# Performance work log

Measured on AMD Instinct MI355X. Metric: run time of the kernel, lower is better.

## Reference

```python
import jax, jax.numpy as jnp
import numpy as np

N = 50000   # active sparse voxels
B = 4       # batch size
FIN = 64
FOUT = 128
TEMB = 256
K = 27      # 3x3x3 kernel offsets
EPS = 1e-5


def _bn(x, gamma, beta, mean, var):
    # inference-style BatchNorm over channel dim
    return (x - mean) * jax.lax.rsqrt(var + EPS) * gamma + beta


def _sparse_conv(feats, nbr, mask, W):
    # submanifold sparse conv via kernel map:
    # out[n] = sum_k mask[k,n] * feats[nbr[k,n]] @ W[k]
    g = feats[nbr] * mask[..., None].astype(feats.dtype)   # [K, N, Fin]
    return jnp.einsum('knf,kfo->no', g, W)                  # [N, Fout]


def _make_kernel_map(k_nbr, k_msk, n):
    nbr = jax.random.randint(k_nbr, (K, N), 0, n, dtype=jnp.int32)
    mask = jax.random.bernoulli(k_msk, 0.4, (K, N))
    # center offset is the identity map and always valid (submanifold conv)
    nbr = nbr.at[K // 2].set(jnp.arange(N, dtype=jnp.int32))
    mask = mask.at[K // 2].set(True)
    return nbr, mask


def setup_inputs() -> dict:
    key = jax.random.key(0)
    ks = jax.random.split(key, 20)
    x_feats = jax.random.normal(ks[0], (N, FIN), jnp.float32)
    batch_idx = jax.random.randint(ks[1], (N,), 0, B, dtype=jnp.int32)
    t = jax.random.normal(ks[2], (B, TEMB), jnp.float32)
    nbr1, mask1 = _make_kernel_map(ks[3], ks[4], N)
    nbr2, mask2 = _make_kernel_map(ks[5], ks[6], N)
    s1 = 1.0 / np.sqrt(FIN * K)
    s2 = 1.0 / np.sqrt(FOUT * K)
    return {
        'x_feats': x_feats, 'batch_idx': batch_idx, 't': t,
        'nbr1': nbr1, 'mask1': mask1, 'nbr2': nbr2, 'mask2': mask2,
        'bn1_gamma': jnp.ones((FIN,), jnp.float32),
        'bn1_beta': jnp.zeros((FIN,), jnp.float32),
        'bn1_mean': 0.1 * jax.random.normal(ks[7], (FIN,), jnp.float32),
        'bn1_var': jax.random.uniform(ks[8], (FIN,), jnp.float32, 0.5, 1.5),
        'W1': s1 * jax.random.normal(ks[9], (K, FIN, FOUT), jnp.float32),
        't_W': (1.0 / np.sqrt(TEMB)) * jax.random.normal(ks[10], (TEMB, FOUT), jnp.float32),
        't_b': jnp.zeros((FOUT,), jnp.float32),
        'bn2_gamma': jnp.ones((FOUT,), jnp.float32),
        'bn2_beta': jnp.zeros((FOUT,), jnp.float32),
        'bn2_mean': 0.1 * jax.random.normal(ks[11], (FOUT,), jnp.float32),
        'bn2_var': jax.random.uniform(ks[12], (FOUT,), jnp.float32, 0.5, 1.5),
        'W2': s2 * jax.random.normal(ks[13], (K, FOUT, FOUT), jnp.float32),
        'res_W': (1.0 / np.sqrt(FIN)) * jax.random.normal(ks[14], (FIN, FOUT), jnp.float32),
        'res_b': jnp.zeros((FOUT,), jnp.float32),
    }


def reference(x_feats, batch_idx, t, nbr1, mask1, nbr2, mask2,
              bn1_gamma, bn1_beta, bn1_mean, bn1_var, W1,
              t_W, t_b,
              bn2_gamma, bn2_beta, bn2_mean, bn2_var, W2,
              res_W, res_b):
    # conv1 block: BN -> SiLU -> sparse Conv3d
    h = jax.nn.silu(_bn(x_feats, bn1_gamma, bn1_beta, bn1_mean, bn1_var))
    h = _sparse_conv(h, nbr1, mask1, W1)                      # [N, FOUT]
    # FiLM-style time embedding, broadcast per point via batch index
    t_emb = jax.nn.silu(t) @ t_W + t_b                        # [B, FOUT]
    h = h + t_emb[batch_idx]
    # conv2 block
    h2 = jax.nn.silu(_bn(h, bn2_gamma, bn2_beta, bn2_mean, bn2_var))
    h2 = _sparse_conv(h2, nbr2, mask2, W2)                    # [N, FOUT]
    # residual connection (f_in != f_out -> Linear)
    return h2 + (x_feats @ res_W + res_b)
```

## Files before the change

### kernel.cpp

```cpp
#include <hip/hip_runtime.h>


#define EPS 1e-5f

typedef __attribute__((ext_vector_type(8))) short s16x8;
typedef __attribute__((ext_vector_type(4))) float f32x4;
typedef __attribute__((ext_vector_type(4))) unsigned short u16x4;

static __device__ __forceinline__ unsigned short f2bf(float f) {
    union { float f; unsigned u; } v; v.f = f;
    unsigned r = v.u + 0x7fffu + ((v.u >> 16) & 1u);
    return (unsigned short)(r >> 16);
}
static __device__ __forceinline__ float silu_d(float x) {
    return x / (1.f + __expf(-x));
}
static __device__ __forceinline__ void gload_lds16(const void* gsrc, void* ldst) {
    __builtin_amdgcn_global_load_lds(
        (const __attribute__((address_space(1))) unsigned int*)gsrc,
        (__attribute__((address_space(3))) unsigned int*)ldst, 16, 0, 0);
}
static __device__ __forceinline__ int mask_shift(const unsigned char* mask, int NV) {
    size_t base = (size_t)13 * (size_t)NV;
    int v = ((base & 3) == 3) ? 2 : 1;
    return (mask[base + v] == 1) ? 0 : 2;
}

__global__ void k_prep_small(const float* __restrict__ t, const float* __restrict__ tW,
                             const float* __restrict__ tb,
                             const float* __restrict__ g2, const float* __restrict__ b2,
                             const float* __restrict__ m2, const float* __restrict__ v2,
                             float* __restrict__ temb, float* __restrict__ sc,
                             float* __restrict__ sh, int B) {
    int tid = threadIdx.x;
    if (tid < B * 128) {
        int b = tid >> 7, o = tid & 127;
        float s = 0.f;
        for (int e = 0; e < 256; ++e) {
            float tv = t[b * 256 + e];
            s += silu_d(tv) * tW[e * 128 + o];
        }
        temb[tid] = s + tb[o];
    }
    if (tid < 128) {
        float rstd = rsqrtf(v2[tid] + EPS);
        float s1 = g2[tid] * rstd;
        sc[tid] = s1;
        sh[tid] = b2[tid] - m2[tid] * s1;
    }
}

__global__ __launch_bounds__(256) void k_shuffle(
        const float* __restrict__ W1, const float* __restrict__ W2,
        const float* __restrict__ rW,
        unsigned short* __restrict__ W1s, unsigned short* __restrict__ W2s,
        unsigned short* __restrict__ rWs) {
    int tid = blockIdx.x * 256 + threadIdx.x;
    const int n1 = 432 * 512, n2 = 864 * 512, n3 = 16 * 512;
    if (tid < n1) {
        int f = tid >> 9, r = tid & 511, lane = r >> 3, j = r & 7;
        int mt = f & 7, fk = f >> 3, ks = fk & 1, ko = fk >> 1;
        int fin = ks * 32 + (lane >> 4) * 8 + j;
        int fout = mt * 16 + (lane & 15);
        W1s[tid] = f2bf(W1[(ko * 64 + fin) * 128 + fout]);
    } else if (tid < n1 + n2) {
        int e = tid - n1;
        int f = e >> 9, r = e & 511, lane = r >> 3, j = r & 7;
        int mt = f & 7, fk = f >> 3, ks = fk & 3, ko = fk >> 2;
        int fin = ks * 32 + (lane >> 4) * 8 + j;
        int fout = mt * 16 + (lane & 15);
        W2s[e] = f2bf(W2[(ko * 128 + fin) * 128 + fout]);
    } else if (tid < n1 + n2 + n3) {
        int e = tid - n1 - n2;
        int f = e >> 9, r = e & 511, lane = r >> 3, j = r & 7;
        int mt = f & 7, ks = f >> 3;
        int fin = ks * 32 + (lane >> 4) * 8 + j;
        int fout = mt * 16 + (lane & 15);
        rWs[e] = f2bf(rW[fin * 128 + fout]);
    }
}

__global__ __launch_bounds__(256) void k_elem(
        const float* __restrict__ x,
        const float* __restrict__ g1, const float* __restrict__ b1,
        const float* __restrict__ m1, const float* __restrict__ v1,
        unsigned short* __restrict__ h1, int NV) {
    int tid = blockIdx.x * 256 + threadIdx.x;
    if (tid >= NV * 16) return;
    int n = tid >> 4, c = (tid & 15) << 2;
    f32x4 xv = *(const f32x4*)(x + n * 64 + c);
    f32x4 gv = *(const f32x4*)(g1 + c);
    f32x4 bv = *(const f32x4*)(b1 + c);
    f32x4 mv = *(const f32x4*)(m1 + c);
    f32x4 vv = *(const f32x4*)(v1 + c);
    u16x4 ho;
#pragma unroll
    for (int j = 0; j < 4; ++j) {
        float xn = (xv[j] - mv[j]) * rsqrtf(vv[j] + EPS) * gv[j] + bv[j];
        ho[j] = f2bf(silu_d(xn));
    }
    *(u16x4*)(h1 + n * 64 + c) = ho;
}

__global__ __launch_bounds__(512) void k_conv1(
        const unsigned short* __restrict__ h1, const int* __restrict__ nbr,
        const unsigned char* __restrict__ mask, const unsigned short* __restrict__ W1s,
        const float* __restrict__ temb, const int* __restrict__ bidx,
        const float* __restrict__ bn2sc, const float* __restrict__ bn2sh,
        unsigned short* __restrict__ h2in, int NV) {
    __shared__ unsigned short lds0[8192];
    __shared__ unsigned short lds1[8192];
    const int lane = threadIdx.x & 63;
    const int wave = threadIdx.x >> 6;
    const int g = lane >> 4, col = lane & 15;
    const int v = blockIdx.x * 128 + wave * 16 + col;
    const bool vok = v < NV;
    const int msh = mask_shift(mask, NV);

    f32x4 acc[8];
    const f32x4 z4 = {0.f, 0.f, 0.f, 0.f};
#pragma unroll
    for (int m = 0; m < 8; ++m) acc[m] = z4;
    const s16x8 zz = {0, 0, 0, 0, 0, 0, 0, 0};

    auto loadr = [&](int t) -> int {
        if (!vok) return -1;
        int off = t * NV + v;
        int nv = nbr[off];
        bool mm = mask[(size_t)off << msh] != 0;
        return mm ? nv : -1;
    };

    {
        const char* src = (const char*)W1s + (size_t)threadIdx.x * 16;
        char* dst = (char*)lds0 + (size_t)threadIdx.x * 16;
#pragma unroll
        for (int i = 0; i < 2; ++i)
            gload_lds16(src + i * 8192, dst + i * 8192);
    }
    int rA = loadr(0);
    int rN = loadr(1);
    int r0 = rA < 0 ? 0 : rA;
    s16x8 p0 = *(const s16x8*)(h1 + r0 * 64 + 0 * 32 + g * 8);
    s16x8 p1 = *(const s16x8*)(h1 + r0 * 64 + 1 * 32 + g * 8);
    __syncthreads();

    unsigned short* bufc = lds0;
    unsigned short* bufn = lds1;

    for (int t = 0; t < 27; ++t) {
        s16x8 q0, q1;
        int rN2 = -1;
        if (t < 26) {
            const char* src = (const char*)W1s + (size_t)(t + 1) * 16384 + (size_t)threadIdx.x * 16;
            char* dst = (char*)bufn + (size_t)threadIdx.x * 16;
#pragma unroll
            for (int i = 0; i < 2; ++i)
                gload_lds16(src + i * 8192, dst + i * 8192);
            int rn = rN < 0 ? 0 : rN;
            q0 = *(const s16x8*)(h1 + rn * 64 + 0 * 32 + g * 8);
            q1 = *(const s16x8*)(h1 + rn * 64 + 1 * 32 + g * 8);
        }
        if (t < 25) rN2 = loadr(t + 2);
        const bool m = rA >= 0;
        s16x8 b0 = m ? p0 : zz;
        s16x8 b1 = m ? p1 : zz;
        const unsigned short* wp = bufc + lane * 8;
#pragma unroll
        for (int mt = 0; mt < 8; ++mt) {
            s16x8 a = *(const s16x8*)(wp + (0 * 8 + mt) * 512);
            acc[mt] = __builtin_amdgcn_mfma_f32_16x16x32_bf16(a, b0, acc[mt], 0, 0, 0);
        }
#pragma unroll
        for (int mt = 0; mt < 8; ++mt) {
            s16x8 a = *(const s16x8*)(wp + (1 * 8 + mt) * 512);
            acc[mt] = __builtin_amdgcn_mfma_f32_16x16x32_bf16(a, b1, acc[mt], 0, 0, 0);
        }
        if (t < 26) {
            __syncthreads();
            p0 = q0; p1 = q1;
            rA = rN; rN = rN2;
            unsigned short* tmp = bufc; bufc = bufn; bufn = tmp;
        }
    }

    if (vok) {
        int b = bidx[v];
        const float* te = temb + b * 128;
#pragma unroll
        for (int mt = 0; mt < 8; ++mt) {
            int c = mt * 16 + g * 4;
            f32x4 val = acc[mt];
            f32x4 tv = *(const f32x4*)(te + c);
            f32x4 sc = *(const f32x4*)(bn2sc + c);
            f32x4 sh = *(const f32x4*)(bn2sh + c);
            u16x4 o;
#pragma unroll
            for (int j = 0; j < 4; ++j) {
                float zv = (val[j] + tv[j]) * sc[j] + sh[j];
                o[j] = f2bf(silu_d(zv));
            }
            *(u16x4*)(h2in + v * 128 + c) = o;
        }
    }
}

__global__ __launch_bounds__(512) void k_conv2(
        const unsigned short* __restrict__ h2in, const int* __restrict__ nbr,
        const unsigned char* __restrict__ mask, const unsigned short* __restrict__ W2s,
        const float* __restrict__ x, const unsigned short* __restrict__ rWs,
        const float* __restrict__ resb, float* __restrict__ out, int NV) {
    __shared__ unsigned short lds0[8192];
    __shared__ unsigned short lds1[8192];
    const int lane = threadIdx.x & 63;
    const int wave = threadIdx.x >> 6;
    const int g = lane >> 4, col = lane & 15;
    const int v = blockIdx.x * 128 + wave * 16 + col;
    const bool vok = v < NV;
    const int msh = mask_shift(mask, NV);

    f32x4 acc[8];
    const f32x4 z4 = {0.f, 0.f, 0.f, 0.f};
#pragma unroll
    for (int m = 0; m < 8; ++m) acc[m] = z4;
    const s16x8 zz = {0, 0, 0, 0, 0, 0, 0, 0};

    auto loadr = [&](int t) -> int {
        if (!vok) return -1;
        int off = t * NV + v;
        int nv = nbr[off];
        bool mm = mask[(size_t)off << msh] != 0;
        return mm ? nv : -1;
    };

    {
        const char* src = (const char*)W2s + (size_t)threadIdx.x * 16;
        char* dst = (char*)lds0 + (size_t)threadIdx.x * 16;
#pragma unroll
        for (int i = 0; i < 2; ++i)
            gload_lds16(src + i * 8192, dst + i * 8192);
    }
    int rA = loadr(0);
    int rN = loadr(1);
    int r0 = rA < 0 ? 0 : rA;
    s16x8 pA0 = *(const s16x8*)(h2in + r0 * 128 + 0 * 32 + g * 8);
    s16x8 pA1 = *(const s16x8*)(h2in + r0 * 128 + 1 * 32 + g * 8);
    s16x8 pB0 = *(const s16x8*)(h2in + r0 * 128 + 2 * 32 + g * 8);
    s16x8 pB1 = *(const s16x8*)(h2in + r0 * 128 + 3 * 32 + g * 8);

    {
        int rv = vok ? v : 0;
#pragma unroll
        for (int ks = 0; ks < 2; ++ks) {
            f32x4 xa = *(const f32x4*)(x + rv * 64 + ks * 32 + g * 8);
            f32x4 xb = *(const f32x4*)(x + rv * 64 + ks * 32 + g * 8 + 4);
            s16x8 b;
#pragma unroll
            for (int j = 0; j < 4; ++j) {
                b[j]     = (short)f2bf(xa[j]);
                b[j + 4] = (short)f2bf(xb[j]);
            }
            const unsigned short* wp = rWs + ks * 4096 + lane * 8;
#pragma unroll
            for (int mt = 0; mt < 8; ++mt) {
                s16x8 a = *(const s16x8*)(wp + mt * 512);
                acc[mt] = __builtin_amdgcn_mfma_f32_16x16x32_bf16(a, b, acc[mt], 0, 0, 0);
            }
        }
    }
    __syncthreads();

    for (int t = 0; t < 27; ++t) {
        const bool m = rA >= 0;
        const int rn = rN < 0 ? 0 : rN;
        s16x8 qA0, qA1, qB0, qB1;
        int rN2 = -1;

        {
            const char* src = (const char*)W2s + ((size_t)t * 2 + 1) * 16384 + (size_t)threadIdx.x * 16;
            char* dst = (char*)lds1 + (size_t)threadIdx.x * 16;
#pragma unroll
            for (int i = 0; i < 2; ++i)
                gload_lds16(src + i * 8192, dst + i * 8192);
            if (t < 26) {
                qA0 = *(const s16x8*)(h2in + rn * 128 + 0 * 32 + g * 8);
                qA1 = *(const s16x8*)(h2in + rn * 128 + 1 * 32 + g * 8);
            }
            if (t < 25) rN2 = loadr(t + 2);
            s16x8 b0 = m ? pA0 : zz;
            s16x8 b1 = m ? pA1 : zz;
            const unsigned short* wp = lds0 + lane * 8;
#pragma unroll
            for (int mt = 0; mt < 8; ++mt) {
                s16x8 a = *(const s16x8*)(wp + (0 * 8 + mt) * 512);
                acc[mt] = __builtin_amdgcn_mfma_f32_16x16x32_bf16(a, b0, acc[mt], 0, 0, 0);
            }
#pragma unroll
            for (int mt = 0; mt < 8; ++mt) {
                s16x8 a = *(const s16x8*)(wp + (1 * 8 + mt) * 512);
                acc[mt] = __builtin_amdgcn_mfma_f32_16x16x32_bf16(a, b1, acc[mt], 0, 0, 0);
            }
            __syncthreads();
        }

        {
            if (t < 26) {
                const char* src = (const char*)W2s + ((size_t)(t + 1) * 2 + 0) * 16384 + (size_t)threadIdx.x * 16;
                char* dst = (char*)lds0 + (size_t)threadIdx.x * 16;
#pragma unroll
                for (int i = 0; i < 2; ++i)
                    gload_lds16(src + i * 8192, dst + i * 8192);
                qB0 = *(const s16x8*)(h2in + rn * 128 + 2 * 32 + g * 8);
                qB1 = *(const s16x8*)(h2in + rn * 128 + 3 * 32 + g * 8);
            }
            s16x8 b0 = m ? pB0 : zz;
            s16x8 b1 = m ? pB1 : zz;
            const unsigned short* wp = lds1 + lane * 8;
#pragma unroll
            for (int mt = 0; mt < 8; ++mt) {
                s16x8 a = *(const s16x8*)(wp + (0 * 8 + mt) * 512);
                acc[mt] = __builtin_amdgcn_mfma_f32_16x16x32_bf16(a, b0, acc[mt], 0, 0, 0);
            }
#pragma unroll
            for (int mt = 0; mt < 8; ++mt) {
                s16x8 a = *(const s16x8*)(wp + (1 * 8 + mt) * 512);
                acc[mt] = __builtin_amdgcn_mfma_f32_16x16x32_bf16(a, b1, acc[mt], 0, 0, 0);
            }
            __syncthreads();
        }

        pA0 = qA0; pA1 = qA1; pB0 = qB0; pB1 = qB1;
        rA = rN; rN = rN2;
    }

    if (vok) {
#pragma unroll
        for (int mt = 0; mt < 8; ++mt) {
            int c = mt * 16 + g * 4;
            f32x4 rr = acc[mt] + *(const f32x4*)(resb + c);
            *(f32x4*)(out + v * 128 + c) = rr;
        }
    }
}

extern "C" void kernel_launch(void* const* d_in, const int* in_sizes, int n_in,
                              void* d_out, int out_size, void* d_ws, size_t ws_size,
                              hipStream_t stream) {
    const float* x          = (const float*)d_in[0];
    const int* bidx         = (const int*)d_in[1];
    const float* t          = (const float*)d_in[2];
    const int* nbr1         = (const int*)d_in[3];
    const unsigned char* mask1 = (const unsigned char*)d_in[4];
    const int* nbr2         = (const int*)d_in[5];
    const unsigned char* mask2 = (const unsigned char*)d_in[6];
    const float* bn1g       = (const float*)d_in[7];
    const float* bn1b       = (const float*)d_in[8];
    const float* bn1m       = (const float*)d_in[9];
    const float* bn1v       = (const float*)d_in[10];
    const float* W1         = (const float*)d_in[11];
    const float* tW         = (const float*)d_in[12];
    const float* tb         = (const float*)d_in[13];
    const float* bn2g       = (const float*)d_in[14];
    const float* bn2b       = (const float*)d_in[15];
    const float* bn2m       = (const float*)d_in[16];
    const float* bn2v       = (const float*)d_in[17];
    const float* W2         = (const float*)d_in[18];
    const float* rW         = (const float*)d_in[19];
    const float* resb       = (const float*)d_in[20];

    const int NV = in_sizes[0] / 64;
    const int B  = in_sizes[2] / 256;
    float* out = (float*)d_out;

    char* ws = (char*)d_ws;
    size_t o_W1s = 0;
    size_t o_W2s = o_W1s + (size_t)432 * 1024;
    size_t o_rWs = o_W2s + (size_t)864 * 1024;
    size_t o_te  = o_rWs + (size_t)16 * 1024;
    size_t o_sc  = o_te  + (size_t)B * 128 * 4;
    size_t o_sh  = o_sc  + 512;
    size_t o_h1  = o_sh  + 512;
    size_t o_h2  = o_h1  + (size_t)NV * 64 * 2;

    unsigned short* W1s  = (unsigned short*)(ws + o_W1s);
    unsigned short* W2s  = (unsigned short*)(ws + o_W2s);
    unsigned short* rWs  = (unsigned short*)(ws + o_rWs);
    float* temb  = (float*)(ws + o_te);
    float* bn2sc = (float*)(ws + o_sc);
    float* bn2sh = (float*)(ws + o_sh);
    unsigned short* h1   = (unsigned short*)(ws + o_h1);
    unsigned short* h2in = (unsigned short*)(ws + o_h2);

    k_prep_small<<<1, 512, 0, stream>>>(t, tW, tb, bn2g, bn2b, bn2m, bn2v,
                                        temb, bn2sc, bn2sh, B);
    {
        int total = (432 + 864 + 16) * 512;
        int grid = (total + 255) / 256;
        k_shuffle<<<grid, 256, 0, stream>>>(W1, W2, rW, W1s, W2s, rWs);
    }
    {
        int total = NV * 16;
        int grid = (total + 255) / 256;
        k_elem<<<grid, 256, 0, stream>>>(x, bn1g, bn1b, bn1m, bn1v, h1, NV);
    }
    {
        int grid = (NV + 127) / 128;
        k_conv1<<<grid, 512, 0, stream>>>(h1, nbr1, mask1, W1s, temb, bidx,
                                          bn2sc, bn2sh, h2in, NV);
        k_conv2<<<grid, 512, 0, stream>>>(h2in, nbr2, mask2, W2s, x, rWs,
                                          resb, out, NV);
    }
}
```

Measured before the change: 143.2 us.

## Split output channels across two blocks per voxel tile in sparse convs

Each 128-voxel tile is now handled by two blocks, each computing one 64-channel half of the output. The shuffled weight layout is reordered so each half's weights are contiguous, which halves per-block LDS weight traffic and accumulator registers. In conv2 the per-offset K loop is restructured into a single double-buffered stage per offset instead of two half-stages. The goal is more blocks and higher occupancy. The cost is that the neighbor index, mask and feature gathers are duplicated across the two blocks.

Result: slower. 199.3 us (+39.2%).

```diff
diff --git a/kernel.cpp b/kernel.cpp
--- a/kernel.cpp
+++ b/kernel.cpp
@@ -59,16 +59,18 @@
     const int n1 = 432 * 512, n2 = 864 * 512, n3 = 16 * 512;
     if (tid < n1) {
         int f = tid >> 9, r = tid & 511, lane = r >> 3, j = r & 7;
-        int mt = f & 7, fk = f >> 3, ks = fk & 1, ko = fk >> 1;
+        int w = f & 7, mtl = w & 3, ks = w >> 2;
+        int chunk = f >> 3, h = chunk & 1, ko = chunk >> 1;
         int fin = ks * 32 + (lane >> 4) * 8 + j;
-        int fout = mt * 16 + (lane & 15);
+        int fout = h * 64 + mtl * 16 + (lane & 15);
         W1s[tid] = f2bf(W1[(ko * 64 + fin) * 128 + fout]);
     } else if (tid < n1 + n2) {
         int e = tid - n1;
         int f = e >> 9, r = e & 511, lane = r >> 3, j = r & 7;
-        int mt = f & 7, fk = f >> 3, ks = fk & 3, ko = fk >> 2;
+        int w = f & 15, mtl = w & 3, ks = w >> 2;
+        int chunk = f >> 4, h = chunk & 1, ko = chunk >> 1;
         int fin = ks * 32 + (lane >> 4) * 8 + j;
-        int fout = mt * 16 + (lane & 15);
+        int fout = h * 64 + mtl * 16 + (lane & 15);
         W2s[e] = f2bf(W2[(ko * 128 + fin) * 128 + fout]);
     } else if (tid < n1 + n2 + n3) {
         int e = tid - n1 - n2;
@@ -108,19 +110,20 @@
         const float* __restrict__ temb, const int* __restrict__ bidx,
         const float* __restrict__ bn2sc, const float* __restrict__ bn2sh,
         unsigned short* __restrict__ h2in, int NV) {
-    __shared__ unsigned short lds0[8192];
-    __shared__ unsigned short lds1[8192];
+    __shared__ unsigned short lds0[4096];
+    __shared__ unsigned short lds1[4096];
+    const int vb = blockIdx.x >> 1, h = blockIdx.x & 1;
     const int lane = threadIdx.x & 63;
     const int wave = threadIdx.x >> 6;
     const int g = lane >> 4, col = lane & 15;
-    const int v = blockIdx.x * 128 + wave * 16 + col;
+    const int v = vb * 128 + wave * 16 + col;
     const bool vok = v < NV;
     const int msh = mask_shift(mask, NV);
 
-    f32x4 acc[8];
+    f32x4 acc[4];
     const f32x4 z4 = {0.f, 0.f, 0.f, 0.f};
 #pragma unroll
-    for (int m = 0; m < 8; ++m) acc[m] = z4;
+    for (int m = 0; m < 4; ++m) acc[m] = z4;
     const s16x8 zz = {0, 0, 0, 0, 0, 0, 0, 0};
 
     auto loadr = [&](int t) -> int {
@@ -132,11 +135,9 @@
     };
 
     {
-        const char* src = (const char*)W1s + (size_t)threadIdx.x * 16;
+        const char* src = (const char*)W1s + (size_t)h * 8192 + (size_t)threadIdx.x * 16;
         char* dst = (char*)lds0 + (size_t)threadIdx.x * 16;
-#pragma unroll
-        for (int i = 0; i < 2; ++i)
-            gload_lds16(src + i * 8192, dst + i * 8192);
+        gload_lds16(src, dst);
     }
     int rA = loadr(0);
     int rN = loadr(1);
@@ -152,11 +153,9 @@
         s16x8 q0, q1;
         int rN2 = -1;
         if (t < 26) {
-            const char* src = (const char*)W1s + (size_t)(t + 1) * 16384 + (size_t)threadIdx.x * 16;
+            const char* src = (const char*)W1s + ((size_t)(t + 1) * 2 + h) * 8192 + (size_t)threadIdx.x * 16;
             char* dst = (char*)bufn + (size_t)threadIdx.x * 16;
-#pragma unroll
-            for (int i = 0; i < 2; ++i)
-                gload_lds16(src + i * 8192, dst + i * 8192);
+            gload_lds16(src, dst);
             int rn = rN < 0 ? 0 : rN;
             q0 = *(const s16x8*)(h1 + rn * 64 + 0 * 32 + g * 8);
             q1 = *(const s16x8*)(h1 + rn * 64 + 1 * 32 + g * 8);
@@ -167,14 +166,14 @@
         s16x8 b1 = m ? p1 : zz;
         const unsigned short* wp = bufc + lane * 8;
 #pragma unroll
-        for (int mt = 0; mt < 8; ++mt) {
-            s16x8 a = *(const s16x8*)(wp + (0 * 8 + mt) * 512);
-            acc[mt] = __builtin_amdgcn_mfma_f32_16x16x32_bf16(a, b0, acc[mt], 0, 0, 0);
-        }
-#pragma unroll
-        for (int mt = 0; mt < 8; ++mt) {
-            s16x8 a = *(const s16x8*)(wp + (1 * 8 + mt) * 512);
-            acc[mt] = __builtin_amdgcn_mfma_f32_16x16x32_bf16(a, b1, acc[mt], 0, 0, 0);
+        for (int mtl = 0; mtl < 4; ++mtl) {
+            s16x8 a = *(const s16x8*)(wp + (0 * 4 + mtl) * 512);
+            acc[mtl] = __builtin_amdgcn_mfma_f32_16x16x32_bf16(a, b0, acc[mtl], 0, 0, 0);
+        }
+#pragma unroll
+        for (int mtl = 0; mtl < 4; ++mtl) {
+            s16x8 a = *(const s16x8*)(wp + (1 * 4 + mtl) * 512);
+            acc[mtl] = __builtin_amdgcn_mfma_f32_16x16x32_bf16(a, b1, acc[mtl], 0, 0, 0);
         }
         if (t < 26) {
             __syncthreads();
@@ -188,9 +187,9 @@
         int b = bidx[v];
         const float* te = temb + b * 128;
 #pragma unroll
-        for (int mt = 0; mt < 8; ++mt) {
-            int c = mt * 16 + g * 4;
-            f32x4 val = acc[mt];
+        for (int mtl = 0; mtl < 4; ++mtl) {
+            int c = h * 64 + mtl * 16 + g * 4;
+            f32x4 val = acc[mtl];
             f32x4 tv = *(const f32x4*)(te + c);
             f32x4 sc = *(const f32x4*)(bn2sc + c);
             f32x4 sh = *(const f32x4*)(bn2sh + c);
@@ -212,17 +211,18 @@
         const float* __restrict__ resb, float* __restrict__ out, int NV) {
     __shared__ unsigned short lds0[8192];
     __shared__ unsigned short lds1[8192];
+    const int vb = blockIdx.x >> 1, h = blockIdx.x & 1;
     const int lane = threadIdx.x & 63;
     const int wave = threadIdx.x >> 6;
     const int g = lane >> 4, col = lane & 15;
-    const int v = blockIdx.x * 128 + wave * 16 + col;
+    const int v = vb * 128 + wave * 16 + col;
     const bool vok = v < NV;
     const int msh = mask_shift(mask, NV);
 
-    f32x4 acc[8];
+    f32x4 acc[4];
     const f32x4 z4 = {0.f, 0.f, 0.f, 0.f};
 #pragma unroll
-    for (int m = 0; m < 8; ++m) acc[m] = z4;
+    for (int m = 0; m < 4; ++m) acc[m] = z4;
     const s16x8 zz = {0, 0, 0, 0, 0, 0, 0, 0};
 
     auto loadr = [&](int t) -> int {
@@ -234,7 +234,7 @@
     };
 
     {
-        const char* src = (const char*)W2s + (size_t)threadIdx.x * 16;
+        const char* src = (const char*)W2s + (size_t)h * 16384 + (size_t)threadIdx.x * 16;
         char* dst = (char*)lds0 + (size_t)threadIdx.x * 16;
 #pragma unroll
         for (int i = 0; i < 2; ++i)
@@ -243,10 +243,10 @@
     int rA = loadr(0);
     int rN = loadr(1);
     int r0 = rA < 0 ? 0 : rA;
-    s16x8 pA0 = *(const s16x8*)(h2in + r0 * 128 + 0 * 32 + g * 8);
-    s16x8 pA1 = *(const s16x8*)(h2in + r0 * 128 + 1 * 32 + g * 8);
-    s16x8 pB0 = *(const s16x8*)(h2in + r0 * 128 + 2 * 32 + g * 8);
-    s16x8 pB1 = *(const s16x8*)(h2in + r0 * 128 + 3 * 32 + g * 8);
+    s16x8 p0 = *(const s16x8*)(h2in + r0 * 128 + 0 * 32 + g * 8);
+    s16x8 p1 = *(const s16x8*)(h2in + r0 * 128 + 1 * 32 + g * 8);
+    s16x8 p2 = *(const s16x8*)(h2in + r0 * 128 + 2 * 32 + g * 8);
+    s16x8 p3 = *(const s16x8*)(h2in + r0 * 128 + 3 * 32 + g * 8);
 
     {
         int rv = vok ? v : 0;
@@ -260,84 +260,73 @@
                 b[j]     = (short)f2bf(xa[j]);
                 b[j + 4] = (short)f2bf(xb[j]);
             }
-            const unsigned short* wp = rWs + ks * 4096 + lane * 8;
-#pragma unroll
-            for (int mt = 0; mt < 8; ++mt) {
-                s16x8 a = *(const s16x8*)(wp + mt * 512);
-                acc[mt] = __builtin_amdgcn_mfma_f32_16x16x32_bf16(a, b, acc[mt], 0, 0, 0);
+#pragma unroll
+            for (int mtl = 0; mtl < 4; ++mtl) {
+                s16x8 a = *(const s16x8*)(rWs + (ks * 8 + h * 4 + mtl) * 512 + lane * 8);
+                acc[mtl] = __builtin_amdgcn_mfma_f32_16x16x32_bf16(a, b, acc[mtl], 0, 0, 0);
             }
         }
     }
     __syncthreads();
 
+    unsigned short* bufc = lds0;
+    unsigned short* bufn = lds1;
+
     for (int t = 0; t < 27; ++t) {
-        const bool m = rA >= 0;
-        const int rn = rN < 0 ? 0 : rN;
-        s16x8 qA0, qA1, qB0, qB1;
+        s16x8 q0, q1, q2, q3;
         int rN2 = -1;
-
-        {
-            const char* src = (const char*)W2s + ((size_t)t * 2 + 1) * 16384 + (size_t)threadIdx.x * 16;
-            char* dst = (char*)lds1 + (size_t)threadIdx.x * 16;
+        if (t < 26) {
+            const char* src = (const char*)W2s + ((size_t)(t + 1) * 2 + h) * 16384 + (size_t)threadIdx.x * 16;
+            char* dst = (char*)bufn + (size_t)threadIdx.x * 16;
 #pragma unroll
             for (int i = 0; i < 2; ++i)
                 gload_lds16(src + i * 8192, dst + i * 8192);
-            if (t < 26) {
-                qA0 = *(const s16x8*)(h2in + rn * 128 + 0 * 32 + g * 8);
-                qA1 = *(const s16x8*)(h2in + rn * 128 + 1 * 32 + g * 8);
-            }
-            if (t < 25) rN2 = loadr(t + 2);
-            s16x8 b0 = m ? pA0 : zz;
-            s16x8 b1 = m ? pA1 : zz;
-            const unsigned short* wp = lds0 + lane * 8;
-#pragma unroll
-            for (int mt = 0; mt < 8; ++mt) {
-                s16x8 a = *(const s16x8*)(wp + (0 * 8 + mt) * 512);
-                acc[mt] = __builtin_amdgcn_mfma_f32_16x16x32_bf16(a, b0, acc[mt], 0, 0, 0);
-            }
-#pragma unroll
-            for (int mt = 0; mt < 8; ++mt) {
-                s16x8 a = *(const s16x8*)(wp + (1 * 8 + mt) * 512);
-                acc[mt] = __builtin_amdgcn_mfma_f32_16x16x32_bf16(a, b1, acc[mt], 0, 0, 0);
-            }
+            int rn = rN < 0 ? 0 : rN;
+            q0 = *(const s16x8*)(h2in + rn * 128 + 0 * 32 + g * 8);
+            q1 = *(const s16x8*)(h2in + rn * 128 + 1 * 32 + g * 8);
+            q2 = *(const s16x8*)(h2in + rn * 128 + 2 * 32 + g * 8);
+            q3 = *(const s16x8*)(h2in + rn * 128 + 3 * 32 + g * 8);
+        }
+        if (t < 25) rN2 = loadr(t + 2);
+        const bool m = rA >= 0;
+        s16x8 b0 = m ? p0 : zz;
+        s16x8 b1 = m ? p1 : zz;
+        s16x8 b2 = m ? p2 : zz;
+        s16x8 b3 = m ? p3 : zz;
+        const unsigned short* wp = bufc + lane * 8;
+#pragma unroll
+        for (int mtl = 0; mtl < 4; ++mtl) {
+            s16x8 a = *(const s16x8*)(wp + (0 * 4 + mtl) * 512);
+            acc[mtl] = __builtin_amdgcn_mfma_f32_16x16x32_bf16(a, b0, acc[mtl], 0, 0, 0);
+        }
+#pragma unroll
+        for (int mtl = 0; mtl < 4; ++mtl) {
+            s16x8 a = *(const s16x8*)(wp + (1 * 4 + mtl) * 512);
+            acc[mtl] = __builtin_amdgcn_mfma_f32_16x16x32_bf16(a, b1, acc[mtl], 0, 0, 0);
+        }
+#pragma unroll
+        for (int mtl = 0; mtl < 4; ++mtl) {
+            s16x8 a = *(const s16x8*)(wp + (2 * 4 + mtl) * 512);
+            acc[mtl] = __builtin_amdgcn_mfma_f32_16x16x32_bf16(a, b2, acc[mtl], 0, 0, 0);
+        }
+#pragma unroll
+        for (int mtl = 0; mtl < 4; ++mtl) {
+            s16x8 a = *(const s16x8*)(wp + (3 * 4 + mtl) * 512);
+            acc[mtl] = __builtin_amdgcn_mfma_f32_16x16x32_bf16(a, b3, acc[mtl], 0, 0, 0);
+        }
+        if (t < 26) {
             __syncthreads();
-        }
-
-        {
-            if (t < 26) {
-                const char* src = (const char*)W2s + ((size_t)(t + 1) * 2 + 0) * 16384 + (size_t)threadIdx.x * 16;
-                char* dst = (char*)lds0 + (size_t)threadIdx.x * 16;
-#pragma unroll
-                for (int i = 0; i < 2; ++i)
-                    gload_lds16(src + i * 8192, dst + i * 8192);
-                qB0 = *(const s16x8*)(h2in + rn * 128 + 2 * 32 + g * 8);
-                qB1 = *(const s16x8*)(h2in + rn * 128 + 3 * 32 + g * 8);
-            }
-            s16x8 b0 = m ? pB0 : zz;
-            s16x8 b1 = m ? pB1 : zz;
-            const unsigned short* wp = lds1 + lane * 8;
-#pragma unroll
-            for (int mt = 0; mt < 8; ++mt) {
-                s16x8 a = *(const s16x8*)(wp + (0 * 8 + mt) * 512);
-                acc[mt] = __builtin_amdgcn_mfma_f32_16x16x32_bf16(a, b0, acc[mt], 0, 0, 0);
-            }
-#pragma unroll
-            for (int mt = 0; mt < 8; ++mt) {
-                s16x8 a = *(const s16x8*)(wp + (1 * 8 + mt) * 512);
-                acc[mt] = __builtin_amdgcn_mfma_f32_16x16x32_bf16(a, b1, acc[mt], 0, 0, 0);
-            }
-            __syncthreads();
-        }
-
-        pA0 = qA0; pA1 = qA1; pB0 = qB0; pB1 = qB1;
-        rA = rN; rN = rN2;
+            p0 = q0; p1 = q1; p2 = q2; p3 = q3;
+            rA = rN; rN = rN2;
+            unsigned short* tmp = bufc; bufc = bufn; bufn = tmp;
+        }
     }
 
     if (vok) {
 #pragma unroll
-        for (int mt = 0; mt < 8; ++mt) {
-            int c = mt * 16 + g * 4;
-            f32x4 rr = acc[mt] + *(const f32x4*)(resb + c);
+        for (int mtl = 0; mtl < 4; ++mtl) {
+            int c = h * 64 + mtl * 16 + g * 4;
+            f32x4 rr = acc[mtl] + *(const f32x4*)(resb + c);
             *(f32x4*)(out + v * 128 + c) = rr;
         }
     }
@@ -404,10 +393,10 @@
         k_elem<<<grid, 256, 0, stream>>>(x, bn1g, bn1b, bn1m, bn1v, h1, NV);
     }
     {
-        int grid = (NV + 127) / 128;
-        k_conv1<<<grid, 512, 0, stream>>>(h1, nbr1, mask1, W1s, temb, bidx,
-                                          bn2sc, bn2sh, h2in, NV);
-        k_conv2<<<grid, 512, 0, stream>>>(h2in, nbr2, mask2, W2s, x, rWs,
-                                          resb, out, NV);
-    }
-}
+        int NB = (NV + 127) / 128;
+        k_conv1<<<NB * 2, 512, 0, stream>>>(h1, nbr1, mask1, W1s, temb, bidx,
+                                            bn2sc, bn2sh, h2in, NV);
+        k_conv2<<<NB * 2, 512, 0, stream>>>(h2in, nbr2, mask2, W2s, x, rWs,
+                                            resb, out, NV);
+    }
+}
```
